# Performance work log

Measured on AMD Instinct MI355X. Metric: run time of the kernel, lower is better.

## Reference

```python
import jax, jax.numpy as jnp
import numpy as np
from jax.scipy.linalg import expm

LAMBDA_ORTHO = 1.0


def setup_inputs() -> dict:
    key = jax.random.key(0)
    so8_raw = jax.random.normal(key, (524288, 8, 8), dtype=jnp.float32)
    return {"so8_raw": so8_raw}


def reference(so8_raw):
    # A = 0.5 * (P - P^T): skew-symmetric part per 8x8 block
    A = 0.5 * (so8_raw - jnp.swapaxes(so8_raw, -1, -2))
    # R = expm(A), batched over leading dim via vmap
    R = jax.vmap(expm)(A)
    # ||R^T R - I||_F per block, then mean over blocks
    gram = jnp.einsum('nji,njk->nik', R, R)  # R^T R, [N,8,8]
    err = gram - jnp.eye(8, dtype=R.dtype)
    ortho_err = jnp.sqrt(jnp.sum(err * err, axis=(1, 2))).mean()
    return LAMBDA_ORTHO * ortho_err
```

## Files before the change

kernel.cpp:

```cpp
#include <hip/hip_runtime.h>
#include <math.h>

#pragma clang fp contract(off)

typedef float f2 __attribute__((ext_vector_type(2)));

static __device__ __forceinline__ f2 sp(float x) { f2 r; r.x = x; r.y = x; return r; }
#define FMA2(A, B, C) __builtin_elementwise_fma((A), (B), (C))

#define EL(m, i, j) (m[(i)*4 + ((j) >> 1)][(j) & 1])

__device__ __forceinline__ void mm8p(const f2* __restrict__ A,
                                     const f2* __restrict__ B,
                                     f2* __restrict__ C) {
  #pragma unroll
  for (int i = 0; i < 8; ++i) {
    #pragma unroll
    for (int c = 0; c < 4; ++c) {
      f2 s = sp(EL(A, i, 0)) * B[0*4 + c];
      #pragma unroll
      for (int k = 1; k < 8; ++k)
        s = FMA2(sp(EL(A, i, k)), B[k*4 + c], s);
      C[i*4 + c] = s;
    }
  }
}

__global__ __launch_bounds__(256, 1)
void triality_kernel(const float* __restrict__ in, double* __restrict__ acc)
{
  const int t = blockIdx.x * 256 + threadIdx.x;
  const float4* src = (const float4*)(in + (size_t)t * 64);

  float p[64];
  #pragma unroll
  for (int i = 0; i < 16; ++i) {
    float4 q4 = src[i];
    p[4*i+0] = q4.x; p[4*i+1] = q4.y; p[4*i+2] = q4.z; p[4*i+3] = q4.w;
  }

  f2 aa[32];
  #pragma unroll
  for (int i = 0; i < 8; ++i)
    #pragma unroll
    for (int j = 0; j < 8; ++j)
      EL(aa, i, j) = 0.5f * (p[i*8+j] - p[j*8+i]);

  float l1 = 0.0f;
  #pragma unroll
  for (int j = 0; j < 8; ++j) {
    float cs = 0.0f;
    #pragma unroll
    for (int i = 0; i < 8; ++i) cs = cs + fabsf(EL(aa, i, j));
    l1 = fmaxf(l1, cs);
  }

  float fl = floorf(log2f(l1 / 3.925724783138660f));
  int ns = (fl > 0.0f) ? (int)fl : 0;
  if (ns > 0) {
    f2 sc = sp(exp2f((float)(-ns)));
    #pragma unroll
    for (int e = 0; e < 32; ++e) aa[e] = aa[e] * sc;
  }

  f2 a2[32];
  #pragma unroll
  for (int i = 0; i < 8; ++i)
    #pragma unroll
    for (int c = 0; c < 4; ++c) {
      f2 s = sp(EL(aa, i, 0)) * aa[0*4 + c];
      #pragma unroll
      for (int k = 1; k < 8; ++k)
        s = FMA2(sp(EL(aa, i, k)), aa[k*4 + c], s);
      a2[i*4 + c] = s;
    }

  f2 a4[32];
  #pragma unroll
  for (int i = 0; i < 8; ++i)
    #pragma unroll
    for (int c = 0; c < 4; ++c) {
      f2 s = sp(EL(a2, i, 0)) * a2[0*4 + c];
      #pragma unroll
      for (int k = 1; k < 8; ++k)
        s = FMA2(sp(EL(a2, i, k)), a2[k*4 + c], s);
      a4[i*4 + c] = s;
    }

  f2 w6[32];
  #pragma unroll
  for (int i = 0; i < 8; ++i)
    #pragma unroll
    for (int c = 0; c < 4; ++c) {
      f2 s = sp(EL(a4, i, 0)) * a2[0*4 + c];
      #pragma unroll
      for (int k = 1; k < 8; ++k)
        s = FMA2(sp(EL(a4, i, k)), a2[k*4 + c], s);
      w6[i*4 + c] = s;
    }

  f2 vv[32];
  #pragma unroll
  for (int e = 0; e < 32; ++e) {
    f2 x6 = w6[e], x4 = a4[e], x2 = a2[e];
    f2 w = FMA2(sp(1512.0f), x4, x6);
    w = FMA2(sp(277200.0f), x2, w);
    f2 v = FMA2(sp(56.0f), x6, sp(25200.0f) * x4);
    v = FMA2(sp(1995840.0f), x2, v);
    w6[e] = w; vv[e] = v;
  }
  #pragma unroll
  for (int i = 0; i < 8; ++i) {
    EL(w6, i, i) = EL(w6, i, i) + 8648640.0f;
    EL(vv, i, i) = EL(vv, i, i) + 17297280.0f;
  }

  f2 uu[32];
  #pragma unroll
  for (int i = 0; i < 8; ++i)
    #pragma unroll
    for (int c = 0; c < 4; ++c) {
      f2 s = sp(EL(aa, i, 0)) * w6[0*4 + c];
      #pragma unroll
      for (int k = 1; k < 8; ++k)
        s = FMA2(sp(EL(aa, i, k)), w6[k*4 + c], s);
      uu[i*4 + c] = s;
    }

  #pragma unroll
  for (int e = 0; e < 32; ++e) {
    f2 U = uu[e], V = vv[e];
    uu[e] = U + V;
    vv[e] = V - U;
  }
  f2* P = uu;
  f2* Q = vv;

  #pragma unroll
  for (int k = 0; k < 8; ++k) {
    float amax = fabsf(EL(Q, k, k)); int jp = k;
    #pragma unroll
    for (int i = k+1; i < 8; ++i) {
      float av = fabsf(EL(Q, i, k));
      if (av > amax) { amax = av; jp = i; }
    }
    #pragma unroll
    for (int i = k+1; i < 8; ++i) {
      bool d = (jp == i);
      #pragma unroll
      for (int j = 0; j < 8; ++j) {
        float x = EL(Q, k, j), y = EL(Q, i, j);
        EL(Q, k, j) = d ? y : x;
        EL(Q, i, j) = d ? x : y;
        float px = EL(P, k, j), py = EL(P, i, j);
        EL(P, k, j) = d ? py : px;
        EL(P, i, j) = d ? px : py;
      }
    }
    float dk = EL(Q, k, k);
    #pragma unroll
    for (int i = k+1; i < 8; ++i) EL(Q, i, k) = EL(Q, i, k) / dk;
    #pragma unroll
    for (int i = k+1; i < 8; ++i) {
      float lik = EL(Q, i, k);
      #pragma unroll
      for (int j = k+1; j < 8; ++j)
        EL(Q, i, j) = __builtin_fmaf(-lik, EL(Q, k, j), EL(Q, i, j));
      f2 nl = sp(-lik);
      #pragma unroll
      for (int c = 0; c < 4; ++c)
        P[i*4 + c] = FMA2(nl, P[k*4 + c], P[i*4 + c]);
    }
  }

  #pragma unroll
  for (int k = 7; k >= 0; --k) {
    float dk = EL(Q, k, k);
    #pragma unroll
    for (int j = 0; j < 8; ++j) EL(P, k, j) = EL(P, k, j) / dk;
    #pragma unroll
    for (int i = 0; i < k; ++i) {
      f2 nu = sp(-EL(Q, i, k));
      #pragma unroll
      for (int c = 0; c < 4; ++c)
        P[i*4 + c] = FMA2(nu, P[k*4 + c], P[i*4 + c]);
    }
  }

  for (int sq = 0; sq < ns; ++sq) {
    f2 t2[32];
    mm8p(P, P, t2);
    #pragma unroll
    for (int e = 0; e < 32; ++e) P[e] = t2[e];
  }

  f2 s2p = sp(0.0f);
  #pragma unroll
  for (int i = 0; i < 8; ++i) {
    #pragma unroll
    for (int c = 0; c < 4; ++c) {
      f2 g = sp(EL(P, 0, i)) * P[0*4 + c];
      #pragma unroll
      for (int j = 1; j < 8; ++j)
        g = FMA2(sp(EL(P, j, i)), P[j*4 + c], g);
      f2 idv; idv.x = (2*c == i) ? 1.0f : 0.0f; idv.y = (2*c + 1 == i) ? 1.0f : 0.0f;
      f2 e = g - idv;
      s2p = FMA2(e, e, s2p);
    }
  }
  float frob = sqrtf(s2p.x + s2p.y);

  double dv = (double)frob;
  #pragma unroll
  for (int off = 32; off > 0; off >>= 1)
    dv += __shfl_down(dv, off);

  __shared__ double part[4];
  const int lane = threadIdx.x & 63;
  const int wid  = threadIdx.x >> 6;
  if (lane == 0) part[wid] = dv;
  __syncthreads();
  if (threadIdx.x == 0) {
    double s = (part[0] + part[1]) + (part[2] + part[3]);
    atomicAdd(acc, s);
  }
}

__global__ void finalize_kernel(const double* __restrict__ acc,
                                float* __restrict__ out, int nmat)
{
  out[0] = (float)(acc[0] / (double)nmat);
}

extern "C" void kernel_launch(void* const* d_in, const int* in_sizes, int n_in,
                              void* d_out, int out_size, void* d_ws, size_t ws_size,
                              hipStream_t stream) {
  const float* in = (const float*)d_in[0];
  float* out = (float*)d_out;
  double* acc = (double*)d_ws;
  int nmat = in_sizes[0] / 64;
  hipMemsetAsync(d_ws, 0, sizeof(double), stream);
  triality_kernel<<<nmat / 256, 256, 0, stream>>>(in, acc);
  finalize_kernel<<<1, 1, 0, stream>>>(acc, out, nmat);
}
```

Baseline: 216.0 us.

## Exploit symmetry of even powers and Gram matrix; tree-reduce pivot search

```diff
diff --git a/kernel.cpp b/kernel.cpp
--- a/kernel.cpp
+++ b/kernel.cpp
@@ -6,6 +6,7 @@
 typedef float f2 __attribute__((ext_vector_type(2)));
 
 static __device__ __forceinline__ f2 sp(float x) { f2 r; r.x = x; r.y = x; return r; }
+static __device__ __forceinline__ f2 mk2(float x, float y) { f2 r; r.x = x; r.y = y; return r; }
 #define FMA2(A, B, C) __builtin_elementwise_fma((A), (B), (C))
 
 #define EL(m, i, j) (m[(i)*4 + ((j) >> 1)][(j) & 1])
@@ -24,6 +25,27 @@
       C[i*4 + c] = s;
     }
   }
+}
+
+__device__ __forceinline__ void mm8p_sym(const f2* __restrict__ M,
+                                         f2* __restrict__ C) {
+  #pragma unroll
+  for (int c = 0; c < 4; ++c)
+    #pragma unroll
+    for (int i = 0; i <= 2*c + 1; ++i) {
+      f2 s = sp(EL(M, i, 0)) * M[0*4 + c];
+      #pragma unroll
+      for (int k = 1; k < 8; ++k)
+        s = FMA2(sp(EL(M, i, k)), M[k*4 + c], s);
+      C[i*4 + c] = s;
+    }
+  #pragma unroll
+  for (int c = 0; c < 4; ++c)
+    #pragma unroll
+    for (int i = 2*c + 2; i < 8; ++i) {
+      EL(C, i, 2*c)     = EL(C, 2*c,     i);
+      EL(C, i, 2*c + 1) = EL(C, 2*c + 1, i);
+    }
 }
 
 __global__ __launch_bounds__(256, 1)
@@ -63,29 +85,9 @@
     for (int e = 0; e < 32; ++e) aa[e] = aa[e] * sc;
   }
 
-  f2 a2[32];
-  #pragma unroll
-  for (int i = 0; i < 8; ++i)
-    #pragma unroll
-    for (int c = 0; c < 4; ++c) {
-      f2 s = sp(EL(aa, i, 0)) * aa[0*4 + c];
-      #pragma unroll
-      for (int k = 1; k < 8; ++k)
-        s = FMA2(sp(EL(aa, i, k)), aa[k*4 + c], s);
-      a2[i*4 + c] = s;
-    }
-
-  f2 a4[32];
-  #pragma unroll
-  for (int i = 0; i < 8; ++i)
-    #pragma unroll
-    for (int c = 0; c < 4; ++c) {
-      f2 s = sp(EL(a2, i, 0)) * a2[0*4 + c];
-      #pragma unroll
-      for (int k = 1; k < 8; ++k)
-        s = FMA2(sp(EL(a2, i, k)), a2[k*4 + c], s);
-      a4[i*4 + c] = s;
-    }
+  f2 a2[32], a4[32];
+  mm8p_sym(aa, a2);
+  mm8p_sym(a2, a4);
 
   f2 w6[32];
   #pragma unroll
@@ -138,33 +140,47 @@
 
   #pragma unroll
   for (int k = 0; k < 8; ++k) {
-    float amax = fabsf(EL(Q, k, k)); int jp = k;
-    #pragma unroll
-    for (int i = k+1; i < 8; ++i) {
-      float av = fabsf(EL(Q, i, k));
-      if (av > amax) { amax = av; jp = i; }
-    }
-    #pragma unroll
-    for (int i = k+1; i < 8; ++i) {
+    float bv[8]; int bi[8]; int n = 8 - k;
+    #pragma unroll
+    for (int i = 0; i < 8; ++i) {
+      if (i < 8 - k) { bv[i] = fabsf(EL(Q, k + i, k)); bi[i] = k + i; }
+    }
+    #pragma unroll
+    for (int stride = 1; stride < 8; stride <<= 1) {
+      #pragma unroll
+      for (int i = 0; i + stride < 8; i += 2 * stride) {
+        if (i + stride < n) {
+          bool g = bv[i + stride] > bv[i];
+          bv[i] = g ? bv[i + stride] : bv[i];
+          bi[i] = g ? bi[i + stride] : bi[i];
+        }
+      }
+    }
+    int jp = bi[0];
+    #pragma unroll
+    for (int i = k + 1; i < 8; ++i) {
       bool d = (jp == i);
       #pragma unroll
-      for (int j = 0; j < 8; ++j) {
+      for (int j = k; j < 8; ++j) {
         float x = EL(Q, k, j), y = EL(Q, i, j);
         EL(Q, k, j) = d ? y : x;
         EL(Q, i, j) = d ? x : y;
-        float px = EL(P, k, j), py = EL(P, i, j);
-        EL(P, k, j) = d ? py : px;
-        EL(P, i, j) = d ? px : py;
       }
+      #pragma unroll
+      for (int c = 0; c < 4; ++c) {
+        f2 px = P[k*4 + c], py = P[i*4 + c];
+        P[k*4 + c] = d ? py : px;
+        P[i*4 + c] = d ? px : py;
+      }
     }
     float dk = EL(Q, k, k);
     #pragma unroll
-    for (int i = k+1; i < 8; ++i) EL(Q, i, k) = EL(Q, i, k) / dk;
-    #pragma unroll
-    for (int i = k+1; i < 8; ++i) {
+    for (int i = k + 1; i < 8; ++i) EL(Q, i, k) = EL(Q, i, k) / dk;
+    #pragma unroll
+    for (int i = k + 1; i < 8; ++i) {
       float lik = EL(Q, i, k);
       #pragma unroll
-      for (int j = k+1; j < 8; ++j)
+      for (int j = k + 1; j < 8; ++j)
         EL(Q, i, j) = __builtin_fmaf(-lik, EL(Q, k, j), EL(Q, i, j));
       f2 nl = sp(-lik);
       #pragma unroll
@@ -196,16 +212,18 @@
 
   f2 s2p = sp(0.0f);
   #pragma unroll
-  for (int i = 0; i < 8; ++i) {
-    #pragma unroll
-    for (int c = 0; c < 4; ++c) {
+  for (int c = 0; c < 4; ++c) {
+    #pragma unroll
+    for (int i = 0; i <= 2*c + 1; ++i) {
       f2 g = sp(EL(P, 0, i)) * P[0*4 + c];
       #pragma unroll
       for (int j = 1; j < 8; ++j)
         g = FMA2(sp(EL(P, j, i)), P[j*4 + c], g);
-      f2 idv; idv.x = (2*c == i) ? 1.0f : 0.0f; idv.y = (2*c + 1 == i) ? 1.0f : 0.0f;
+      f2 idv = mk2((i == 2*c) ? 1.0f : 0.0f, (i == 2*c + 1) ? 1.0f : 0.0f);
       f2 e = g - idv;
-      s2p = FMA2(e, e, s2p);
+      f2 wv = mk2((i < 2*c) ? 2.0f : (i == 2*c) ? 1.0f : 0.0f,
+                  (i < 2*c + 1) ? 2.0f : 1.0f);
+      s2p = FMA2(wv, e * e, s2p);
     }
   }
   float frob = sqrtf(s2p.x + s2p.y);
```

Measured after the change: 227.8 us. 1.05x slower.
